# Performance work log

Measured on AMD Instinct MI355X. Metric: run time of the kernel, lower is better.

Reference implementation:

```python
import jax, jax.numpy as jnp
import numpy as np

DT = 0.01          # integration timestep
TH_HI = 1.0        # upper firing threshold
TH_LO = -1.0       # lower firing threshold


def setup_inputs() -> dict:
    key = jax.random.key(0)
    inputs = jax.random.normal(key, (64, 256, 1024), dtype=jnp.float32)
    return {"inputs": inputs}


def reference(inputs):
    # inputs: [B, T, D] pre-activation drive at each timestep
    rates = jnp.tanh(inputs)                     # activation(inputs), [B, T, D]
    x = jnp.swapaxes(rates, 0, 1)                # [T, B, D] for scan over time

    def step(v, r):
        v = v + r * DT                           # integrate
        sp = (v >= TH_HI).astype(v.dtype)        # positive spike
        sn = (v <= TH_LO).astype(v.dtype)        # negative spike
        v = v - sp * TH_HI - sn * TH_LO          # subtractive (self-regulating) reset
        out = (sp - sn) / DT                     # signed spike train scaled by 1/dt
        return v, out

    v0 = jnp.zeros(x.shape[1:], dtype=x.dtype)   # initial membrane state
    _, spikes = jax.lax.scan(step, v0, x)        # spikes: [T, B, D]
    spikes = jnp.swapaxes(spikes, 0, 1)          # [B, T, D]

    # spiking-aware (straight-through) output: spikes forward, rates gradient
    out = rates + jax.lax.stop_gradient(spikes - rates)
    return out
```

## Files before the change

### kernel.cpp

```cpp
#include <hip/hip_runtime.h>
#include <stdint.h>

#define B_DIM 64
#define T_STEPS 256
#define D_DIM 1024
#define CT 16
#define CHUNKS (T_STEPS / CT)
#define TPB 256

__device__ __forceinline__ float xla_tanhf(float x) {
    const float kClamp = 7.90531110763549805f;
    float xc = fminf(fmaxf(x, -kClamp), kClamp);
    float x2 = xc * xc;
    float p = __builtin_fmaf(x2, -2.76076847742355e-16f, 2.00018790482477e-13f);
    p = __builtin_fmaf(x2, p, -8.60467152213735e-11f);
    p = __builtin_fmaf(x2, p, 5.12229709037114e-08f);
    p = __builtin_fmaf(x2, p, 1.48572235717979e-05f);
    p = __builtin_fmaf(x2, p, 6.37261928875436e-04f);
    p = __builtin_fmaf(x2, p, 4.89352455891786e-03f);
    p = xc * p;
    float q = __builtin_fmaf(x2, 1.19825839466702e-06f, 1.18534705686654e-04f);
    q = __builtin_fmaf(x2, q, 2.26843463243900e-03f);
    q = __builtin_fmaf(x2, q, 4.89352518554385e-03f);
    float r = p / q;
    return (fabsf(x) < 0.0004f) ? x : r;
}

#define LD(i) "global_load_dword %" #i ", %16, %17\n\t" \
              "v_add_u32 %16, 0x1000, %16\n\t"

#define ISSUE16(B) asm volatile( \
    LD(0) LD(1) LD(2) LD(3) LD(4) LD(5) LD(6) LD(7) \
    LD(8) LD(9) LD(10) LD(11) LD(12) LD(13) LD(14) LD(15) \
    : "=v"(B[0]), "=v"(B[1]), "=v"(B[2]), "=v"(B[3]), \
      "=v"(B[4]), "=v"(B[5]), "=v"(B[6]), "=v"(B[7]), \
      "=v"(B[8]), "=v"(B[9]), "=v"(B[10]), "=v"(B[11]), \
      "=v"(B[12]), "=v"(B[13]), "=v"(B[14]), "=v"(B[15]), \
      "+v"(voffi) \
    : "s"(inp_u) : "memory")

#define WAITBUF(B, CNT) asm volatile("s_waitcnt vmcnt(" CNT ")" \
    : "+v"(B[0]), "+v"(B[1]), "+v"(B[2]), "+v"(B[3]), \
      "+v"(B[4]), "+v"(B[5]), "+v"(B[6]), "+v"(B[7]), \
      "+v"(B[8]), "+v"(B[9]), "+v"(B[10]), "+v"(B[11]), \
      "+v"(B[12]), "+v"(B[13]), "+v"(B[14]), "+v"(B[15]) \
    :: "memory")

#define COMPUTE16(B) \
    _Pragma("unroll") \
    for (int u = 0; u < CT; ++u) { \
        float r = xla_tanhf(B[u]); \
        v = __builtin_fmaf(r, 0.01f, v); \
        float sp = (v >= 1.0f)  ? 1.0f : 0.0f; \
        float sn = (v <= -1.0f) ? 1.0f : 0.0f; \
        v = (v - sp) + sn; \
        float o = (sp - sn) * 100.0f; \
        asm volatile("global_store_dword %0, %1, %2 nt\n\t" \
                     "v_add_u32 %0, 0x1000, %0" \
                     : "+v"(voffo) : "v"(o), "s"(outp_u) : "memory"); \
    }

#define CHUNK_MID(CUR, NXT) do { ISSUE16(NXT); WAITBUF(CUR, "32"); COMPUTE16(CUR); } while (0)

__global__ __launch_bounds__(TPB)
void spike_scan_kernel(const float* __restrict__ in, float* __restrict__ out) {
    const int gid = blockIdx.x * blockDim.x + threadIdx.x;
    const int b = gid >> 10;
    const int d = gid & (D_DIM - 1);
    const uint32_t base_bytes = ((uint32_t)b * (T_STEPS * D_DIM) + (uint32_t)d) * 4u;

    uint32_t voffi = base_bytes;
    uint32_t voffo = base_bytes;
    const uint64_t inp_u  = (uint64_t)in;
    const uint64_t outp_u = (uint64_t)out;

    float bufA[CT], bufB[CT];
    float v = 0.0f;

    ISSUE16(bufA);
    ISSUE16(bufB); WAITBUF(bufA, "16"); COMPUTE16(bufA);
    CHUNK_MID(bufB, bufA);
    #pragma unroll 1
    for (int c2 = 1; c2 <= 6; ++c2) {
        CHUNK_MID(bufA, bufB);
        CHUNK_MID(bufB, bufA);
    }
    CHUNK_MID(bufA, bufB);
    WAITBUF(bufB, "16"); COMPUTE16(bufB);
}

extern "C" void kernel_launch(void* const* d_in, const int* in_sizes, int n_in,
                              void* d_out, int out_size, void* d_ws, size_t ws_size,
                              hipStream_t stream) {
    const float* in = (const float*)d_in[0];
    float* out = (float*)d_out;
    dim3 block(TPB);
    dim3 grid((B_DIM * D_DIM) / TPB);
    spike_scan_kernel<<<grid, block, 0, stream>>>(in, out);
}
```

Measured before the change: 112.2 us.

## Triple-buffer input prefetch, batch tanh per chunk, and drop nt store hint

Raises the software pipeline from two to three 16-step load buffers, so two chunks of loads are in flight while one chunk is computed. The vmcnt wait thresholds are adjusted to match the new issue order. Within each chunk, all 16 tanh evaluations are now computed before the serial membrane scan, which gives more independent work to overlap. The nontemporal hint on output stores is removed. With only about one wave per SIMD, the kernel depends on hiding memory latency. The extra buffer raises VGPR use, and the hand-counted waits rely on stores and loads being counted together in vmcnt.

```diff
diff --git a/kernel.cpp b/kernel.cpp
--- a/kernel.cpp
+++ b/kernel.cpp
@@ -29,38 +29,41 @@
 #define LD(i) "global_load_dword %" #i ", %16, %17\n\t" \
               "v_add_u32 %16, 0x1000, %16\n\t"
 
-#define ISSUE16(B) asm volatile( \
+#define ISSUE16(Bf) asm volatile( \
     LD(0) LD(1) LD(2) LD(3) LD(4) LD(5) LD(6) LD(7) \
     LD(8) LD(9) LD(10) LD(11) LD(12) LD(13) LD(14) LD(15) \
-    : "=v"(B[0]), "=v"(B[1]), "=v"(B[2]), "=v"(B[3]), \
-      "=v"(B[4]), "=v"(B[5]), "=v"(B[6]), "=v"(B[7]), \
-      "=v"(B[8]), "=v"(B[9]), "=v"(B[10]), "=v"(B[11]), \
-      "=v"(B[12]), "=v"(B[13]), "=v"(B[14]), "=v"(B[15]), \
+    : "=v"(Bf[0]), "=v"(Bf[1]), "=v"(Bf[2]), "=v"(Bf[3]), \
+      "=v"(Bf[4]), "=v"(Bf[5]), "=v"(Bf[6]), "=v"(Bf[7]), \
+      "=v"(Bf[8]), "=v"(Bf[9]), "=v"(Bf[10]), "=v"(Bf[11]), \
+      "=v"(Bf[12]), "=v"(Bf[13]), "=v"(Bf[14]), "=v"(Bf[15]), \
       "+v"(voffi) \
     : "s"(inp_u) : "memory")
 
-#define WAITBUF(B, CNT) asm volatile("s_waitcnt vmcnt(" CNT ")" \
-    : "+v"(B[0]), "+v"(B[1]), "+v"(B[2]), "+v"(B[3]), \
-      "+v"(B[4]), "+v"(B[5]), "+v"(B[6]), "+v"(B[7]), \
-      "+v"(B[8]), "+v"(B[9]), "+v"(B[10]), "+v"(B[11]), \
-      "+v"(B[12]), "+v"(B[13]), "+v"(B[14]), "+v"(B[15]) \
+#define WAITBUF(Bf, CNT) asm volatile("s_waitcnt vmcnt(" CNT ")" \
+    : "+v"(Bf[0]), "+v"(Bf[1]), "+v"(Bf[2]), "+v"(Bf[3]), \
+      "+v"(Bf[4]), "+v"(Bf[5]), "+v"(Bf[6]), "+v"(Bf[7]), \
+      "+v"(Bf[8]), "+v"(Bf[9]), "+v"(Bf[10]), "+v"(Bf[11]), \
+      "+v"(Bf[12]), "+v"(Bf[13]), "+v"(Bf[14]), "+v"(Bf[15]) \
     :: "memory")
 
-#define COMPUTE16(B) \
+#define COMPUTE16(Bf) do { \
+    float rr[CT]; \
+    _Pragma("unroll") \
+    for (int u = 0; u < CT; ++u) rr[u] = xla_tanhf(Bf[u]); \
     _Pragma("unroll") \
     for (int u = 0; u < CT; ++u) { \
-        float r = xla_tanhf(B[u]); \
-        v = __builtin_fmaf(r, 0.01f, v); \
+        v = __builtin_fmaf(rr[u], 0.01f, v); \
         float sp = (v >= 1.0f)  ? 1.0f : 0.0f; \
         float sn = (v <= -1.0f) ? 1.0f : 0.0f; \
         v = (v - sp) + sn; \
         float o = (sp - sn) * 100.0f; \
-        asm volatile("global_store_dword %0, %1, %2 nt\n\t" \
+        asm volatile("global_store_dword %0, %1, %2\n\t" \
                      "v_add_u32 %0, 0x1000, %0" \
                      : "+v"(voffo) : "v"(o), "s"(outp_u) : "memory"); \
-    }
+    } \
+} while (0)
 
-#define CHUNK_MID(CUR, NXT) do { ISSUE16(NXT); WAITBUF(CUR, "32"); COMPUTE16(CUR); } while (0)
+#define CHUNK_MID(CUR, NXT) do { ISSUE16(NXT); WAITBUF(CUR, "48"); COMPUTE16(CUR); } while (0)
 
 __global__ __launch_bounds__(TPB)
 void spike_scan_kernel(const float* __restrict__ in, float* __restrict__ out) {
@@ -74,19 +77,22 @@
     const uint64_t inp_u  = (uint64_t)in;
     const uint64_t outp_u = (uint64_t)out;
 
-    float bufA[CT], bufB[CT];
+    float bufA[CT], bufB[CT], bufC[CT];
     float v = 0.0f;
 
     ISSUE16(bufA);
-    ISSUE16(bufB); WAITBUF(bufA, "16"); COMPUTE16(bufA);
+    ISSUE16(bufB);
+    ISSUE16(bufC);
+    WAITBUF(bufA, "32"); COMPUTE16(bufA);
+    #pragma unroll 1
+    for (int it = 0; it < 4; ++it) {
+        CHUNK_MID(bufB, bufA);
+        CHUNK_MID(bufC, bufB);
+        CHUNK_MID(bufA, bufC);
+    }
     CHUNK_MID(bufB, bufA);
-    #pragma unroll 1
-    for (int c2 = 1; c2 <= 6; ++c2) {
-        CHUNK_MID(bufA, bufB);
-        CHUNK_MID(bufB, bufA);
-    }
-    CHUNK_MID(bufA, bufB);
-    WAITBUF(bufB, "16"); COMPUTE16(bufB);
+    WAITBUF(bufC, "32"); COMPUTE16(bufC);
+    WAITBUF(bufA, "16"); COMPUTE16(bufA);
 }
 
 extern "C" void kernel_launch(void* const* d_in, const int* in_sizes, int n_in,
```

New measurement: 114.3 us. About the same (+1.9%).
